# Kernel tuning notes

Measured on AMD Instinct MI355X. Metric: run time of the kernel, lower is better.

Reference implementation:

```python
import jax, jax.numpy as jnp
import numpy as np

DIM = 64
HEADS = 8
P = 4  # polarizations
EPS = 1e-12


def _conv2d(x, w, b, groups):
    # x: [N,C,H,W], w: [O, C//groups, kh, kw] (torch OIHW), stride 1, SAME padding
    y = jax.lax.conv_general_dilated(
        x, w, window_strides=(1, 1), padding='SAME',
        dimension_numbers=('NCHW', 'OIHW', 'NCHW'), feature_group_count=groups)
    return y + b[None, :, None, None]


def setup_inputs() -> dict:
    key = jax.random.key(0)
    ks = jax.random.split(key, 12)
    B, C, H, W = 4, DIM, 128, 128
    s = 1.0 / np.sqrt(C)
    x_in = jax.random.normal(ks[0], (B * P, C, H, W), dtype=jnp.float32)
    mask = jax.random.uniform(ks[1], (B * P, C, H, W), dtype=jnp.float32)
    wq = jax.random.normal(ks[2], (C, C), dtype=jnp.float32) * s
    wk = jax.random.normal(ks[3], (C, C), dtype=jnp.float32) * s
    wv = jax.random.normal(ks[4], (C, C), dtype=jnp.float32) * s
    w_proj = jax.random.normal(ks[5], (C, C), dtype=jnp.float32) * s
    b_proj = jax.random.normal(ks[6], (C,), dtype=jnp.float32) * 0.01
    rescale = jnp.ones((HEADS, 1, 1), dtype=jnp.float32)
    dw_w = jax.random.normal(ks[7], (C, 1, 3, 3), dtype=jnp.float32) * (1.0 / 3.0)
    dw_b = jax.random.normal(ks[8], (C,), dtype=jnp.float32) * 0.01
    pw_w = jax.random.normal(ks[9], (C, C, 1, 1), dtype=jnp.float32) * s
    pw_b = jax.random.normal(ks[10], (C,), dtype=jnp.float32) * 0.01
    return {'x_in': x_in, 'mask': mask, 'wq': wq, 'wk': wk, 'wv': wv,
            'w_proj': w_proj, 'b_proj': b_proj, 'rescale': rescale,
            'dw_w': dw_w, 'dw_b': dw_b, 'pw_w': pw_w, 'pw_b': pw_b}


def reference(x_in, mask, wq, wk, wv, w_proj, b_proj, rescale, dw_w, dw_b, pw_w, pw_b):
    bp, c, h, w = x_in.shape
    b_num = bp // P
    dh = c // HEADS
    # 'b p c h w -> (b h w) p c'
    x = x_in.reshape(b_num, P, c, h, w).transpose(0, 3, 4, 1, 2).reshape(b_num * h * w, P, c)
    # torch Linear (no bias): x @ W.T
    q = jnp.einsum('bpc,dc->bpd', x, wq)
    k = jnp.einsum('bpc,dc->bpd', x, wk)
    v = jnp.einsum('bpc,dc->bpd', x, wv)
    # 'b p (h c) -> b h p c'
    q = q.reshape(-1, P, HEADS, dh).transpose(0, 2, 1, 3)
    k = k.reshape(-1, P, HEADS, dh).transpose(0, 2, 1, 3)
    v = v.reshape(-1, P, HEADS, dh).transpose(0, 2, 1, 3)
    # L2 normalize along head dim (torch F.normalize: clamp_min(eps))
    q = q / jnp.maximum(jnp.linalg.norm(q, axis=-1, keepdims=True), EPS)
    k = k / jnp.maximum(jnp.linalg.norm(k, axis=-1, keepdims=True), EPS)
    atten = jnp.einsum('bhpc,bhqc->bhpq', q, k) * rescale  # rescale: [heads,1,1]
    # mask branch: depthwise 3x3 -> GELU(exact) -> pointwise 1x1
    mg = _conv2d(mask, dw_w, dw_b, groups=c)
    mg = jax.nn.gelu(mg, approximate=False)
    mg = _conv2d(mg, pw_w, pw_b, groups=1)
    mg = mg.reshape(b_num, P, c, h, w).mean(axis=2)  # [b,p,h,w]
    mb = mg.transpose(0, 2, 3, 1).reshape(b_num * h * w, P)  # '(b h w) p'
    mask_bias = mb[:, None, :] - mb[:, :, None]  # [B, p, p]
    atten = atten + mask_bias[:, None, :, :]
    atten = jax.nn.softmax(atten, axis=-1)
    out = jnp.einsum('bhpq,bhqc->bhpc', atten, v)
    out = out.transpose(0, 2, 1, 3).reshape(-1, P, c)  # 'b h p c -> b p (h c)'
    out = jnp.einsum('bpc,dc->bpd', out, w_proj) + b_proj
    # '(b h w) p c -> b p c h w' -> [(b p), c, h, w]
    out = out.reshape(b_num, h, w, P, c).transpose(0, 3, 4, 1, 2)
    return out.reshape(b_num * P, c, h, w)
```

## Files before the change

kernel.cpp:

```cpp
#include <hip/hip_runtime.h>
#include <hip/hip_bf16.h>

#define HSZ 128
#define WSZ 128
#define HWSZ (HSZ*WSZ)
#define NB 4

#define OFF_MB 0

typedef unsigned short u16;
typedef __attribute__((ext_vector_type(8))) short bf16x8;
typedef __attribute__((ext_vector_type(4))) float f32x4;

__device__ __forceinline__ float bf2f(u16 u) {
    return __uint_as_float(((unsigned int)u) << 16);
}
__device__ __forceinline__ unsigned int cvt_pk_bf16(float lo, float hi) {
    __hip_bfloat162 h = __float22bfloat162_rn(make_float2(lo, hi));
    return *(unsigned int*)&h;
}
__device__ __forceinline__ int sswz(int s) { return s ^ (s >> 3); }
__device__ __forceinline__ bf16x8 load_bfrag(const float* W, int drow, int k0) {
    float4 a = *(const float4*)(W + drow*64 + k0);
    float4 b = *(const float4*)(W + drow*64 + k0 + 4);
    unsigned int u[4];
    u[0] = cvt_pk_bf16(a.x, a.y); u[1] = cvt_pk_bf16(a.z, a.w);
    u[2] = cvt_pk_bf16(b.x, b.y); u[3] = cvt_pk_bf16(b.z, b.w);
    return *(bf16x8*)u;
}

__global__ __launch_bounds__(1024) void mask_kernel(const float* __restrict__ mask,
                                                    const float* __restrict__ dww,
                                                    const float* __restrict__ dwb,
                                                    const float* __restrict__ pww,
                                                    float* __restrict__ ws) {
    __shared__ float red[4][256][4];
    __shared__ float cmS[64];
    int tid = threadIdx.x;
    if (tid < 64) {
        float s = 0.f;
        for (int co = 0; co < 64; ++co) s += pww[co*64 + tid];
        cmS[tid] = s * (1.0f/64.0f);
    }
    __syncthreads();
    int bid = blockIdx.x;
    int bp = bid >> 4;
    int hg = bid & 15;
    int cq = tid >> 8;
    int t = tid & 255;
    int h = hg*8 + (t >> 5);
    int w0 = (t & 31) << 2;
    const float* mb_ = mask + (size_t)bp*64*HWSZ;
    int hm = h > 0 ? h-1 : 0;
    int hp = h < 127 ? h+1 : 127;
    float vt = h > 0 ? 1.f : 0.f;
    float vb = h < 127 ? 1.f : 0.f;
    float vl = w0 > 0 ? 1.f : 0.f;
    float vr = w0 < 124 ? 1.f : 0.f;
    int wl = w0 > 0 ? w0-1 : 0;
    int wr = w0 < 124 ? w0+4 : 127;
    float acc0=0.f, acc1=0.f, acc2=0.f, acc3=0.f;
    for (int ci = 0; ci < 16; ++ci) {
        int c = cq*16 + ci;
        const float* rc = mb_ + c*HWSZ;
        const float* r0 = rc + hm*WSZ;
        const float* r1 = rc + h*WSZ;
        const float* r2 = rc + hp*WSZ;
        float4 m0 = *(const float4*)(r0 + w0);
        float4 m1 = *(const float4*)(r1 + w0);
        float4 m2 = *(const float4*)(r2 + w0);
        float L0 = r0[wl]*vl, L1 = r1[wl]*vl, L2 = r2[wl]*vl;
        float R0 = r0[wr]*vr, R1 = r1[wr]*vr, R2 = r2[wr]*vr;
        float w00 = dww[c*9+0]*vt, w01 = dww[c*9+1]*vt, w02 = dww[c*9+2]*vt;
        float w10 = dww[c*9+3],    w11 = dww[c*9+4],    w12 = dww[c*9+5];
        float w20 = dww[c*9+6]*vb, w21 = dww[c*9+7]*vb, w22 = dww[c*9+8]*vb;
        float bb = dwb[c];
        float s0 = bb + w00*L0   + w01*m0.x + w02*m0.y
                      + w10*L1   + w11*m1.x + w12*m1.y
                      + w20*L2   + w21*m2.x + w22*m2.y;
        float s1 = bb + w00*m0.x + w01*m0.y + w02*m0.z
                      + w10*m1.x + w11*m1.y + w12*m1.z
                      + w20*m2.x + w21*m2.y + w22*m2.z;
        float s2 = bb + w00*m0.y + w01*m0.z + w02*m0.w
                      + w10*m1.y + w11*m1.z + w12*m1.w
                      + w20*m2.y + w21*m2.z + w22*m2.w;
        float s3 = bb + w00*m0.z + w01*m0.w + w02*R0
                      + w10*m1.z + w11*m1.w + w12*R1
                      + w20*m2.z + w21*m2.w + w22*R2;
        float cmc = cmS[c];
        acc0 += cmc * (0.5f*s0*(1.f + erff(s0*0.70710678118654752f)));
        acc1 += cmc * (0.5f*s1*(1.f + erff(s1*0.70710678118654752f)));
        acc2 += cmc * (0.5f*s2*(1.f + erff(s2*0.70710678118654752f)));
        acc3 += cmc * (0.5f*s3*(1.f + erff(s3*0.70710678118654752f)));
    }
    red[cq][t][0] = acc0;
    red[cq][t][1] = acc1;
    red[cq][t][2] = acc2;
    red[cq][t][3] = acc3;
    __syncthreads();
    if (tid < 256) {
        int b = bp >> 2, p = bp & 3;
        size_t base = (size_t)b*HWSZ + h*WSZ + w0;
        #pragma unroll
        for (int e = 0; e < 4; ++e) {
            float v = red[0][tid][e] + red[1][tid][e] + red[2][tid][e] + red[3][tid][e];
            ws[OFF_MB + (base+e)*4 + p] = v;
        }
    }
}

__global__ __launch_bounds__(1024, 8) void attn_kernel(const float* __restrict__ x_in,
                                                       const float* __restrict__ wq,
                                                       const float* __restrict__ wk,
                                                       const float* __restrict__ wv,
                                                       const float* __restrict__ wp,
                                                       const float* __restrict__ bpj,
                                                       const float* __restrict__ rsc,
                                                       const float* __restrict__ ws,
                                                       float* __restrict__ out) {
    __shared__ u16 smem[32768];
    u16* ldsA = smem;
    u16* ldsQ = smem + 8192;
    u16* ldsK = smem + 16384;
    u16* ldsV = smem + 24576;
    unsigned int* ldsA32 = (unsigned int*)ldsA;

    int t = threadIdx.x;
    int lane = t & 63;
    int wid = __builtin_amdgcn_readfirstlane(t >> 6);
    int dq = wid & 3;
    int mh = wid >> 2;
    int n15 = lane & 15;
    int quad = lane >> 4;
    int b = blockIdx.x >> 9;
    int hw0 = (blockIdx.x & 511) << 5;

    bf16x8 fq0 = load_bfrag(wq, dq*16 + n15, quad*8);
    bf16x8 fq1 = load_bfrag(wq, dq*16 + n15, 32 + quad*8);
    bf16x8 fk0 = load_bfrag(wk, dq*16 + n15, quad*8);
    bf16x8 fk1 = load_bfrag(wk, dq*16 + n15, 32 + quad*8);
    bf16x8 fv0 = load_bfrag(wv, dq*16 + n15, quad*8);
    bf16x8 fv1 = load_bfrag(wv, dq*16 + n15, 32 + quad*8);

    {
        int rp = t >> 3, l4 = t & 7;
        int p = rp >> 5, cp = rp & 31;
        int c0 = cp*2;
        const float* r0 = x_in + (size_t)(b*256 + p*64 + c0)*HWSZ + hw0 + l4*4;
        float4 v0 = *(const float4*)r0;
        float4 v1 = *(const float4*)(r0 + HWSZ);
        int kt = c0 >> 5, qd = (c0 >> 3) & 3, j2 = (c0 & 7) >> 1;
        float a0v[4] = {v0.x, v0.y, v0.z, v0.w};
        float a1v[4] = {v1.x, v1.y, v1.z, v1.w};
        #pragma unroll
        for (int e = 0; e < 4; ++e) {
            int tau = (p << 5) + (l4 << 2) + e;
            int slot = (tau & 15) | (qd << 4);
            ldsA32[((tau >> 4)*2 + kt)*256 + sswz(slot)*4 + j2] = cvt_pk_bf16(a0v[e], a1v[e]);
        }
    }
    __syncthreads();

    int sl8 = sswz(lane)*8;
    for (int m = 0; m < 2; ++m) {
        int mt = mh*2 + m;
        bf16x8 a0 = *(const bf16x8*)(ldsA + mt*1024 + sl8);
        bf16x8 a1 = *(const bf16x8*)(ldsA + mt*1024 + 512 + sl8);
        f32x4 aq = {0.f,0.f,0.f,0.f};
        f32x4 ak = {0.f,0.f,0.f,0.f};
        f32x4 av = {0.f,0.f,0.f,0.f};
        aq = __builtin_amdgcn_mfma_f32_16x16x32_bf16(fq0, a0, aq, 0, 0, 0);
        aq = __builtin_amdgcn_mfma_f32_16x16x32_bf16(fq1, a1, aq, 0, 0, 0);
        ak = __builtin_amdgcn_mfma_f32_16x16x32_bf16(fk0, a0, ak, 0, 0, 0);
        ak = __builtin_amdgcn_mfma_f32_16x16x32_bf16(fk1, a1, ak, 0, 0, 0);
        av = __builtin_amdgcn_mfma_f32_16x16x32_bf16(fv0, a0, av, 0, 0, 0);
        av = __builtin_amdgcn_mfma_f32_16x16x32_bf16(fv1, a1, av, 0, 0, 0);
        int tg = mt*16 + n15;
        int tok = (tg & 31)*4 + (tg >> 5);
        int base = dq*4 + quad;
        int X = n15 & 7;
        int g = (base & 1) | ((((base >> 1) ^ X) & 7) << 1);
        int off = tok*64 + g*4;
        uint2 pq, pk, pv;
        pq.x = cvt_pk_bf16(aq[0], aq[1]); pq.y = cvt_pk_bf16(aq[2], aq[3]);
        pk.x = cvt_pk_bf16(ak[0], ak[1]); pk.y = cvt_pk_bf16(ak[2], ak[3]);
        pv.x = cvt_pk_bf16(av[0], av[1]); pv.y = cvt_pk_bf16(av[2], av[3]);
        *(uint2*)(ldsQ + off) = pq;
        *(uint2*)(ldsK + off) = pk;
        *(uint2*)(ldsV + off) = pv;
    }
    __syncthreads();

    {
        int p = t & 3;
        int hd = (t >> 2) & 7;
        int pix = t >> 5;
        int tok = pix*4 + p;
        int off = tok*64 + ((hd ^ (pix & 7)) << 3);
        bf16x8 q8 = *(const bf16x8*)(ldsQ + off);
        bf16x8 k8 = *(const bf16x8*)(ldsK + off);
        bf16x8 v8 = *(const bf16x8*)(ldsV + off);
        float qv[8], kv[8];
        float sq = 0.f, sk = 0.f;
        #pragma unroll
        for (int j = 0; j < 8; ++j) {
            qv[j] = bf2f((u16)q8[j]);
            kv[j] = bf2f((u16)k8[j]);
            sq += qv[j]*qv[j];
            sk += kv[j]*kv[j];
        }
        float iq = rsqrtf(fmaxf(sq, 1e-24f));
        float ik = rsqrtf(fmaxf(sk, 1e-24f));
        float d0 = 0.f, d1 = 0.f, d2 = 0.f, d3 = 0.f;
        #pragma unroll
        for (int j = 0; j < 8; ++j) {
            float kj = kv[j];
            d0 += qv[j]*kj;
            d1 += qv[j]*__shfl_xor(kj, 1);
            d2 += qv[j]*__shfl_xor(kj, 2);
            d3 += qv[j]*__shfl_xor(kj, 3);
        }
        float mbp = ws[OFF_MB + ((size_t)b*HWSZ + hw0 + pix)*4 + p];
        float iqrs = iq * rsc[hd];
        float s0 = d0*(iqrs*ik)                 + mbp;
        float s1 = d1*(iqrs*__shfl_xor(ik, 1))  + __shfl_xor(mbp, 1);
        float s2 = d2*(iqrs*__shfl_xor(ik, 2))  + __shfl_xor(mbp, 2);
        float s3 = d3*(iqrs*__shfl_xor(ik, 3))  + __shfl_xor(mbp, 3);
        float mx = fmaxf(fmaxf(s0, s1), fmaxf(s2, s3));
        float e0 = __expf(s0-mx), e1 = __expf(s1-mx);
        float e2 = __expf(s2-mx), e3 = __expf(s3-mx);
        float inv = 1.0f / (e0+e1+e2+e3);
        float w0 = e0*inv, w1 = e1*inv, w2 = e2*inv, w3 = e3*inv;
        float y[8];
        #pragma unroll
        for (int j = 0; j < 8; ++j) {
            float vj = bf2f((u16)v8[j]);
            y[j] = w0*vj + w1*__shfl_xor(vj, 1)
                 + w2*__shfl_xor(vj, 2) + w3*__shfl_xor(vj, 3);
        }
        int tau = (p << 5) + pix;
        unsigned int pk4[4];
        pk4[0] = cvt_pk_bf16(y[0], y[1]); pk4[1] = cvt_pk_bf16(y[2], y[3]);
        pk4[2] = cvt_pk_bf16(y[4], y[5]); pk4[3] = cvt_pk_bf16(y[6], y[7]);
        int slot = (tau & 15) | ((hd & 3) << 4);
        *(uint4*)(ldsA32 + ((tau >> 4)*2 + (hd >> 2))*256 + sswz(slot)*4) = *(uint4*)pk4;
    }
    __syncthreads();

    bf16x8 fp0 = load_bfrag(wp, dq*16 + n15, quad*8);
    bf16x8 fp1 = load_bfrag(wp, dq*16 + n15, 32 + quad*8);
    float4 b4 = *(const float4*)(bpj + dq*16 + quad*4);
    for (int m = 0; m < 2; ++m) {
        int mt = mh*2 + m;
        bf16x8 a0 = *(const bf16x8*)(ldsA + mt*1024 + sl8);
        bf16x8 a1 = *(const bf16x8*)(ldsA + mt*1024 + 512 + sl8);
        f32x4 ao = {0.f,0.f,0.f,0.f};
        ao = __builtin_amdgcn_mfma_f32_16x16x32_bf16(fp0, a0, ao, 0, 0, 0);
        ao = __builtin_amdgcn_mfma_f32_16x16x32_bf16(fp1, a1, ao, 0, 0, 0);
        int px = m*16 + n15;
        size_t obase = ((size_t)((b*4 + mh)*64 + dq*16 + quad*4))*HWSZ + hw0 + px;
        out[obase]          = ao[0] + b4.x;
        out[obase +   HWSZ] = ao[1] + b4.y;
        out[obase + 2*HWSZ] = ao[2] + b4.z;
        out[obase + 3*HWSZ] = ao[3] + b4.w;
    }
}

extern "C" void kernel_launch(void* const* d_in, const int* in_sizes, int n_in,
                              void* d_out, int out_size, void* d_ws, size_t ws_size,
                              hipStream_t stream) {
    const float* x_in  = (const float*)d_in[0];
    const float* mask  = (const float*)d_in[1];
    const float* wq    = (const float*)d_in[2];
    const float* wk    = (const float*)d_in[3];
    const float* wv    = (const float*)d_in[4];
    const float* wproj = (const float*)d_in[5];
    const float* bproj = (const float*)d_in[6];
    const float* resc  = (const float*)d_in[7];
    const float* dww   = (const float*)d_in[8];
    const float* dwb   = (const float*)d_in[9];
    const float* pww   = (const float*)d_in[10];
    float* ws = (float*)d_ws;
    float* outp = (float*)d_out;

    hipLaunchKernelGGL(mask_kernel, dim3(256), dim3(1024), 0, stream,
                       mask, dww, dwb, pww, ws);
    hipLaunchKernelGGL(attn_kernel, dim3(2048), dim3(1024), 0, stream,
                       x_in, wq, wk, wv, wproj, bproj, resc, ws, outp);
}
```

Measured before the change: 261.2 us.

## Halve attention block size, reuse LDS buffers, and use DPP quad permutes

The attention kernel now runs 512 threads per block instead of 1024, so each wave handles four m-tiles and each thread handles two pixels. LDS shrinks from 64KB to 48KB by staging V in registers and overwriting the input tile and Q buffer, which costs extra barriers. Cross-lane exchanges inside each quad switch from __shfl_xor to DPP quad_perm moves. Projection weights are loaded up front. The aim is to fit more blocks per CU and make the lane exchanges cheaper, at the price of higher register pressure and more synchronization.

```diff
diff --git a/kernel.cpp b/kernel.cpp
--- a/kernel.cpp
+++ b/kernel.cpp
@@ -20,6 +20,15 @@
     return *(unsigned int*)&h;
 }
 __device__ __forceinline__ int sswz(int s) { return s ^ (s >> 3); }
+__device__ __forceinline__ float qp1(float x) {
+    return __uint_as_float(__builtin_amdgcn_mov_dpp(__float_as_uint(x), 0xB1, 0xF, 0xF, false));
+}
+__device__ __forceinline__ float qp2(float x) {
+    return __uint_as_float(__builtin_amdgcn_mov_dpp(__float_as_uint(x), 0x4E, 0xF, 0xF, false));
+}
+__device__ __forceinline__ float qp3(float x) {
+    return __uint_as_float(__builtin_amdgcn_mov_dpp(__float_as_uint(x), 0x1B, 0xF, 0xF, false));
+}
 __device__ __forceinline__ bf16x8 load_bfrag(const float* W, int drow, int k0) {
     float4 a = *(const float4*)(W + drow*64 + k0);
     float4 b = *(const float4*)(W + drow*64 + k0 + 4);
@@ -109,27 +118,27 @@
     }
 }
 
-__global__ __launch_bounds__(1024, 8) void attn_kernel(const float* __restrict__ x_in,
-                                                       const float* __restrict__ wq,
-                                                       const float* __restrict__ wk,
-                                                       const float* __restrict__ wv,
-                                                       const float* __restrict__ wp,
-                                                       const float* __restrict__ bpj,
-                                                       const float* __restrict__ rsc,
-                                                       const float* __restrict__ ws,
-                                                       float* __restrict__ out) {
-    __shared__ u16 smem[32768];
-    u16* ldsA = smem;
-    u16* ldsQ = smem + 8192;
-    u16* ldsK = smem + 16384;
-    u16* ldsV = smem + 24576;
-    unsigned int* ldsA32 = (unsigned int*)ldsA;
+__global__ __launch_bounds__(512, 6) void attn_kernel(const float* __restrict__ x_in,
+                                                      const float* __restrict__ wq,
+                                                      const float* __restrict__ wk,
+                                                      const float* __restrict__ wv,
+                                                      const float* __restrict__ wp,
+                                                      const float* __restrict__ bpj,
+                                                      const float* __restrict__ rsc,
+                                                      const float* __restrict__ ws,
+                                                      float* __restrict__ out) {
+    __shared__ u16 smem[24576];
+    u16* ldsAV = smem;
+    u16* ldsQ  = smem + 8192;
+    u16* ldsK  = smem + 16384;
+    unsigned int* ldsAV32 = (unsigned int*)ldsAV;
+    unsigned int* ldsQ32  = (unsigned int*)ldsQ;
 
     int t = threadIdx.x;
     int lane = t & 63;
     int wid = __builtin_amdgcn_readfirstlane(t >> 6);
     int dq = wid & 3;
-    int mh = wid >> 2;
+    int half = wid >> 2;
     int n15 = lane & 15;
     int quad = lane >> 4;
     int b = blockIdx.x >> 9;
@@ -141,9 +150,13 @@
     bf16x8 fk1 = load_bfrag(wk, dq*16 + n15, 32 + quad*8);
     bf16x8 fv0 = load_bfrag(wv, dq*16 + n15, quad*8);
     bf16x8 fv1 = load_bfrag(wv, dq*16 + n15, 32 + quad*8);
-
-    {
-        int rp = t >> 3, l4 = t & 7;
+    bf16x8 fp0 = load_bfrag(wp, dq*16 + n15, quad*8);
+    bf16x8 fp1 = load_bfrag(wp, dq*16 + n15, 32 + quad*8);
+    float4 b4 = *(const float4*)(bpj + dq*16 + quad*4);
+
+    for (int it = 0; it < 2; ++it) {
+        int i = t + (it << 9);
+        int rp = i >> 3, l4 = i & 7;
         int p = rp >> 5, cp = rp & 31;
         int c0 = cp*2;
         const float* r0 = x_in + (size_t)(b*256 + p*64 + c0)*HWSZ + hw0 + l4*4;
@@ -156,16 +169,18 @@
         for (int e = 0; e < 4; ++e) {
             int tau = (p << 5) + (l4 << 2) + e;
             int slot = (tau & 15) | (qd << 4);
-            ldsA32[((tau >> 4)*2 + kt)*256 + sswz(slot)*4 + j2] = cvt_pk_bf16(a0v[e], a1v[e]);
+            ldsAV32[((tau >> 4)*2 + kt)*256 + sswz(slot)*4 + j2] = cvt_pk_bf16(a0v[e], a1v[e]);
         }
     }
     __syncthreads();
 
     int sl8 = sswz(lane)*8;
-    for (int m = 0; m < 2; ++m) {
-        int mt = mh*2 + m;
-        bf16x8 a0 = *(const bf16x8*)(ldsA + mt*1024 + sl8);
-        bf16x8 a1 = *(const bf16x8*)(ldsA + mt*1024 + 512 + sl8);
+    uint2 vreg[4];
+    #pragma unroll
+    for (int m = 0; m < 4; ++m) {
+        int mt = half*4 + m;
+        bf16x8 a0 = *(const bf16x8*)(ldsAV + mt*1024 + sl8);
+        bf16x8 a1 = *(const bf16x8*)(ldsAV + mt*1024 + 512 + sl8);
         f32x4 aq = {0.f,0.f,0.f,0.f};
         f32x4 ak = {0.f,0.f,0.f,0.f};
         f32x4 av = {0.f,0.f,0.f,0.f};
@@ -181,25 +196,39 @@
         int X = n15 & 7;
         int g = (base & 1) | ((((base >> 1) ^ X) & 7) << 1);
         int off = tok*64 + g*4;
-        uint2 pq, pk, pv;
+        uint2 pq, pk;
         pq.x = cvt_pk_bf16(aq[0], aq[1]); pq.y = cvt_pk_bf16(aq[2], aq[3]);
         pk.x = cvt_pk_bf16(ak[0], ak[1]); pk.y = cvt_pk_bf16(ak[2], ak[3]);
-        pv.x = cvt_pk_bf16(av[0], av[1]); pv.y = cvt_pk_bf16(av[2], av[3]);
         *(uint2*)(ldsQ + off) = pq;
         *(uint2*)(ldsK + off) = pk;
-        *(uint2*)(ldsV + off) = pv;
-    }
-    __syncthreads();
-
-    {
-        int p = t & 3;
-        int hd = (t >> 2) & 7;
-        int pix = t >> 5;
-        int tok = pix*4 + p;
+        vreg[m].x = cvt_pk_bf16(av[0], av[1]);
+        vreg[m].y = cvt_pk_bf16(av[2], av[3]);
+    }
+    __syncthreads();
+    #pragma unroll
+    for (int m = 0; m < 4; ++m) {
+        int tg = (half*4 + m)*16 + n15;
+        int tok = (tg & 31)*4 + (tg >> 5);
+        int base = dq*4 + quad;
+        int X = n15 & 7;
+        int g = (base & 1) | ((((base >> 1) ^ X) & 7) << 1);
+        *(uint2*)(ldsAV + tok*64 + g*4) = vreg[m];
+    }
+    __syncthreads();
+
+    uint4 yreg[2];
+    int p2 = t & 3;
+    int hd = (t >> 2) & 7;
+    int pix0 = t >> 5;
+    float rs = rsc[hd];
+    #pragma unroll
+    for (int u = 0; u < 2; ++u) {
+        int pix = pix0 + u*16;
+        int tok = pix*4 + p2;
         int off = tok*64 + ((hd ^ (pix & 7)) << 3);
         bf16x8 q8 = *(const bf16x8*)(ldsQ + off);
         bf16x8 k8 = *(const bf16x8*)(ldsK + off);
-        bf16x8 v8 = *(const bf16x8*)(ldsV + off);
+        bf16x8 v8 = *(const bf16x8*)(ldsAV + off);
         float qv[8], kv[8];
         float sq = 0.f, sk = 0.f;
         #pragma unroll
@@ -216,16 +245,16 @@
         for (int j = 0; j < 8; ++j) {
             float kj = kv[j];
             d0 += qv[j]*kj;
-            d1 += qv[j]*__shfl_xor(kj, 1);
-            d2 += qv[j]*__shfl_xor(kj, 2);
-            d3 += qv[j]*__shfl_xor(kj, 3);
-        }
-        float mbp = ws[OFF_MB + ((size_t)b*HWSZ + hw0 + pix)*4 + p];
-        float iqrs = iq * rsc[hd];
-        float s0 = d0*(iqrs*ik)                 + mbp;
-        float s1 = d1*(iqrs*__shfl_xor(ik, 1))  + __shfl_xor(mbp, 1);
-        float s2 = d2*(iqrs*__shfl_xor(ik, 2))  + __shfl_xor(mbp, 2);
-        float s3 = d3*(iqrs*__shfl_xor(ik, 3))  + __shfl_xor(mbp, 3);
+            d1 += qv[j]*qp1(kj);
+            d2 += qv[j]*qp2(kj);
+            d3 += qv[j]*qp3(kj);
+        }
+        float mbp = ws[OFF_MB + ((size_t)b*HWSZ + hw0 + pix)*4 + p2];
+        float iqrs = iq * rs;
+        float s0 = d0*(iqrs*ik)      + mbp;
+        float s1 = d1*(iqrs*qp1(ik)) + qp1(mbp);
+        float s2 = d2*(iqrs*qp2(ik)) + qp2(mbp);
+        float s3 = d3*(iqrs*qp3(ik)) + qp3(mbp);
         float mx = fmaxf(fmaxf(s0, s1), fmaxf(s2, s3));
         float e0 = __expf(s0-mx), e1 = __expf(s1-mx);
         float e2 = __expf(s2-mx), e3 = __expf(s3-mx);
@@ -235,30 +264,34 @@
         #pragma unroll
         for (int j = 0; j < 8; ++j) {
             float vj = bf2f((u16)v8[j]);
-            y[j] = w0*vj + w1*__shfl_xor(vj, 1)
-                 + w2*__shfl_xor(vj, 2) + w3*__shfl_xor(vj, 3);
-        }
-        int tau = (p << 5) + pix;
-        unsigned int pk4[4];
-        pk4[0] = cvt_pk_bf16(y[0], y[1]); pk4[1] = cvt_pk_bf16(y[2], y[3]);
-        pk4[2] = cvt_pk_bf16(y[4], y[5]); pk4[3] = cvt_pk_bf16(y[6], y[7]);
+            y[j] = w0*vj + w1*qp1(vj) + w2*qp2(vj) + w3*qp3(vj);
+        }
+        yreg[u].x = cvt_pk_bf16(y[0], y[1]);
+        yreg[u].y = cvt_pk_bf16(y[2], y[3]);
+        yreg[u].z = cvt_pk_bf16(y[4], y[5]);
+        yreg[u].w = cvt_pk_bf16(y[6], y[7]);
+    }
+    __syncthreads();
+    #pragma unroll
+    for (int u = 0; u < 2; ++u) {
+        int pix = pix0 + u*16;
+        int tau = (p2 << 5) + pix;
         int slot = (tau & 15) | ((hd & 3) << 4);
-        *(uint4*)(ldsA32 + ((tau >> 4)*2 + (hd >> 2))*256 + sswz(slot)*4) = *(uint4*)pk4;
-    }
-    __syncthreads();
-
-    bf16x8 fp0 = load_bfrag(wp, dq*16 + n15, quad*8);
-    bf16x8 fp1 = load_bfrag(wp, dq*16 + n15, 32 + quad*8);
-    float4 b4 = *(const float4*)(bpj + dq*16 + quad*4);
-    for (int m = 0; m < 2; ++m) {
-        int mt = mh*2 + m;
-        bf16x8 a0 = *(const bf16x8*)(ldsA + mt*1024 + sl8);
-        bf16x8 a1 = *(const bf16x8*)(ldsA + mt*1024 + 512 + sl8);
+        *(uint4*)(ldsQ32 + ((tau >> 4)*2 + (hd >> 2))*256 + sswz(slot)*4) = yreg[u];
+    }
+    __syncthreads();
+
+    #pragma unroll
+    for (int m = 0; m < 4; ++m) {
+        int mt = half*4 + m;
+        bf16x8 a0 = *(const bf16x8*)(ldsQ + mt*1024 + sl8);
+        bf16x8 a1 = *(const bf16x8*)(ldsQ + mt*1024 + 512 + sl8);
         f32x4 ao = {0.f,0.f,0.f,0.f};
         ao = __builtin_amdgcn_mfma_f32_16x16x32_bf16(fp0, a0, ao, 0, 0, 0);
         ao = __builtin_amdgcn_mfma_f32_16x16x32_bf16(fp1, a1, ao, 0, 0, 0);
-        int px = m*16 + n15;
-        size_t obase = ((size_t)((b*4 + mh)*64 + dq*16 + quad*4))*HWSZ + hw0 + px;
+        int p = mt >> 1;
+        int px = (mt & 1)*16 + n15;
+        size_t obase = ((size_t)((b*4 + p)*64 + dq*16 + quad*4))*HWSZ + hw0 + px;
         out[obase]          = ao[0] + b4.x;
         out[obase +   HWSZ] = ao[1] + b4.y;
         out[obase + 2*HWSZ] = ao[2] + b4.z;
@@ -285,6 +318,6 @@
 
     hipLaunchKernelGGL(mask_kernel, dim3(256), dim3(1024), 0, stream,
                        mask, dww, dwb, pww, ws);
-    hipLaunchKernelGGL(attn_kernel, dim3(2048), dim3(1024), 0, stream,
+    hipLaunchKernelGGL(attn_kernel, dim3(2048), dim3(512), 0, stream,
                        x_in, wq, wk, wv, wproj, bproj, resc, ws, outp);
 }
```

Measured after the change: 240.9 us. 1.08x faster.
